# Kernel optimization log

Measured on AMD Instinct MI355X. Metric: run time of the kernel, lower is better.

The kernel has to match this reference:

```python
import jax, jax.numpy as jnp
import numpy as np

HIDDEN = 4096
N_HEADS = 32
N_KV_HEADS = 8
HEAD_DIM = HIDDEN // N_HEADS  # 128
GROUPS = N_HEADS // N_KV_HEADS  # 4
ROPE_BASE = 10000.0
BATCH, SEQ = 1, 2048


def _rope_cos_sin(position_ids, dim, base):
    # position_ids: [b, s] int -> cos/sin [b, s, dim]
    inv_freq = 1.0 / (base ** (jnp.arange(0, dim, 2, dtype=jnp.float32) / dim))  # [dim/2]
    freqs = position_ids.astype(jnp.float32)[..., None] * inv_freq  # [b, s, dim/2]
    emb = jnp.concatenate([freqs, freqs], axis=-1)  # [b, s, dim]
    return jnp.cos(emb), jnp.sin(emb)


def _rotate_half(x):
    x1, x2 = jnp.split(x, 2, axis=-1)
    return jnp.concatenate([-x2, x1], axis=-1)


def setup_inputs() -> dict:
    key = jax.random.key(0)
    ks = jax.random.split(key, 8)
    s = 0.02
    return {
        'hidden_states': jax.random.normal(ks[0], (BATCH, SEQ, HIDDEN), dtype=jnp.float32),
        'position_ids': jnp.broadcast_to(jnp.arange(SEQ, dtype=jnp.int64), (BATCH, SEQ)),
        'Wq': jax.random.normal(ks[1], (HIDDEN, N_HEADS * HEAD_DIM), dtype=jnp.float32) * s,
        'bq': jax.random.normal(ks[2], (N_HEADS * HEAD_DIM,), dtype=jnp.float32) * s,
        'Wk': jax.random.normal(ks[3], (HIDDEN, N_KV_HEADS * HEAD_DIM), dtype=jnp.float32) * s,
        'bk': jax.random.normal(ks[4], (N_KV_HEADS * HEAD_DIM,), dtype=jnp.float32) * s,
        'Wv': jax.random.normal(ks[5], (HIDDEN, N_KV_HEADS * HEAD_DIM), dtype=jnp.float32) * s,
        'bv': jax.random.normal(ks[6], (N_KV_HEADS * HEAD_DIM,), dtype=jnp.float32) * s,
        'Wo': jax.random.normal(ks[7], (HIDDEN, HIDDEN), dtype=jnp.float32) * s,
    }


def reference(hidden_states, position_ids, Wq, bq, Wk, bk, Wv, bv, Wo):
    b, s, _ = hidden_states.shape
    # QKV projections (bias=True for q/k/v per module)
    q = hidden_states @ Wq + bq  # [b, s, H*d]
    k = hidden_states @ Wk + bk  # [b, s, Hk*d]
    v = hidden_states @ Wv + bv  # [b, s, Hk*d]
    q = q.reshape(b, s, N_HEADS, HEAD_DIM)
    k = k.reshape(b, s, N_KV_HEADS, HEAD_DIM)
    v = v.reshape(b, s, N_KV_HEADS, HEAD_DIM)

    # RoPE gathered by position_ids
    cos, sin = _rope_cos_sin(position_ids, HEAD_DIM, ROPE_BASE)  # [b, s, d]
    cos = cos[:, :, None, :]
    sin = sin[:, :, None, :]
    q = q * cos + _rotate_half(q) * sin
    k = k * cos + _rotate_half(k) * sin

    # GQA causal attention: group query heads over shared kv heads
    qg = q.reshape(b, s, N_KV_HEADS, GROUPS, HEAD_DIM)
    scale = 1.0 / jnp.sqrt(jnp.asarray(HEAD_DIM, dtype=q.dtype))
    scores = jnp.einsum('bqhgd,bkhd->bhgqk', qg, k) * scale  # [b, Hk, g, s, s]
    causal = jnp.tril(jnp.ones((s, s), dtype=bool))
    scores = jnp.where(causal, scores, jnp.finfo(scores.dtype).min)
    probs = jax.nn.softmax(scores, axis=-1)
    out = jnp.einsum('bhgqk,bkhd->bqhgd', probs, v)  # [b, s, Hk, g, d]
    out = out.reshape(b, s, HIDDEN)
    return out @ Wo  # o_proj, bias=False
```

## Files before the change

kernel.cpp:

```cpp
#include <hip/hip_runtime.h>
#include <hip/hip_bf16.h>

typedef __hip_bfloat16 bf16;
typedef __attribute__((ext_vector_type(8))) __bf16 bf16x8;
typedef __attribute__((ext_vector_type(4))) float f32x4;

#define SEQ 2048
#define HID 4096
#define NH 32
#define NKV 8
#define HD 128
#define KVDIM 1024
#define QKVN 6144

#define MiB (1024 * 1024)
#define SCALE_LOG2E 0.12751743f

__device__ __forceinline__ void gl_lds16(const void* g, void* lds) {
  __builtin_amdgcn_global_load_lds((const __attribute__((address_space(1))) void*)g,
                                   (__attribute__((address_space(3))) void*)lds,
                                   16, 0, 0);
}

__device__ __forceinline__ float unplo(unsigned u) { return __uint_as_float(u << 16); }
__device__ __forceinline__ float unphi(unsigned u) { return __uint_as_float(u & 0xffff0000u); }
__device__ __forceinline__ unsigned packbf(float a, float b) {
  bf16 t[2] = {__float2bfloat16(a), __float2bfloat16(b)};
  return *reinterpret_cast<unsigned*>(t);
}

__global__ void transpose_all_kernel(const float* __restrict__ Wq, const float* __restrict__ Wk,
                                     const float* __restrict__ Wv, const float* __restrict__ Wo,
                                     bf16* __restrict__ Wqkvt, bf16* __restrict__ Wot,
                                     const float* __restrict__ hidden, bf16* __restrict__ Xb,
                                     const float* __restrict__ bq, const float* __restrict__ bk,
                                     const float* __restrict__ bv, float* __restrict__ bqkv) {
  __shared__ float tile[64][65];
  int t = blockIdx.x;
  int tx = threadIdx.x, ty = threadIdx.y;
  int tid = ty * 64 + tx;
  if (t >= 18432) {
    int i = (t - 18432) * 256 + tid;
    bqkv[i] = (i < HID) ? bq[i] : (i < HID + KVDIM ? bk[i - HID] : bv[i - HID - KVDIM]);
    return;
  }
  if (t >= 10240) {
    int i = ((t - 10240) * 256 + tid) * 4;
    float4 v = *reinterpret_cast<const float4*>(hidden + i);
    bf16 o[4] = {__float2bfloat16(v.x), __float2bfloat16(v.y),
                 __float2bfloat16(v.z), __float2bfloat16(v.w)};
    *reinterpret_cast<short4*>(Xb + i) = *reinterpret_cast<const short4*>(o);
    return;
  }
  const float* in;
  bf16* out;
  int si, xt, yt;
  if (t < 4096)      { in = Wq; out = Wqkvt;                           si = HID;   xt = t & 63; yt = t >> 6; }
  else if (t < 5120) { t -= 4096; in = Wk; out = Wqkvt + (size_t)HID * HID;           si = KVDIM; xt = t & 15; yt = t >> 4; }
  else if (t < 6144) { t -= 5120; in = Wv; out = Wqkvt + (size_t)(HID + KVDIM) * HID; si = KVDIM; xt = t & 15; yt = t >> 4; }
  else               { t -= 6144; in = Wo; out = Wot;                 si = HID;   xt = t & 63; yt = t >> 6; }
  int c0 = xt * 64, r0 = yt * 64;
#pragma unroll
  for (int i = 0; i < 64; i += 4)
    tile[ty + i][tx] = in[(size_t)(r0 + ty + i) * si + (c0 + tx)];
  __syncthreads();
#pragma unroll
  for (int i = 0; i < 64; i += 4)
    out[(size_t)(c0 + ty + i) * HID + (r0 + tx)] = __float2bfloat16(tile[tx][ty + i]);
}

__global__ void postqkv_kernel(const bf16* __restrict__ Ch, bf16* __restrict__ Qb,
                               bf16* __restrict__ Kb, bf16* __restrict__ Vt) {
  __shared__ float tile[32][33];
  int b = blockIdx.x;
  int tid = threadIdx.x;
  if (b < 10240) {
    bool isQ = (b < 8192);
    int idx = (isQ ? b : b - 8192) * 256 + tid;
    int j = idx & 31;
    int h = (idx >> 5) & (isQ ? 31 : 7);
    int s = idx >> (isQ ? 10 : 8);
    size_t bi = (size_t)s * QKVN + (isQ ? 0 : HID) + h * HD;
    unsigned u1 = *reinterpret_cast<const unsigned*>(Ch + bi + 2 * j);
    unsigned u2 = *reinterpret_cast<const unsigned*>(Ch + bi + 64 + 2 * j);
    float x1a = unplo(u1), x1b = unphi(u1);
    float x2a = unplo(u2), x2b = unphi(u2);
    float inv0 = __expf(-(float)(2 * j) * 0.14391156831212787f);
    float inv1 = __expf(-(float)(2 * j + 1) * 0.14391156831212787f);
    float sn0, cs0, sn1, cs1;
    __sincosf((float)s * inv0, &sn0, &cs0);
    __sincosf((float)s * inv1, &sn1, &cs1);
    if (isQ) {
      cs0 *= SCALE_LOG2E; sn0 *= SCALE_LOG2E;
      cs1 *= SCALE_LOG2E; sn1 *= SCALE_LOG2E;
    }
    size_t bo = (size_t)s * (isQ ? HID : KVDIM) + h * HD;
    bf16* Ob = isQ ? Qb : Kb;
    *reinterpret_cast<unsigned*>(Ob + bo + 2 * j) =
        packbf(x1a * cs0 - x2a * sn0, x1b * cs1 - x2b * sn1);
    *reinterpret_cast<unsigned*>(Ob + bo + 64 + 2 * j) =
        packbf(x2a * cs0 + x1a * sn0, x2b * cs1 + x1b * sn1);
  } else {
    int t = b - 10240;
    int xt = t & 31, yt = t >> 5;
    int tx = tid & 31, ty = tid >> 5;
#pragma unroll
    for (int i = 0; i < 32; i += 8)
      tile[ty + i][tx] = __bfloat162float(Ch[(size_t)(yt * 32 + ty + i) * QKVN + (HID + KVDIM) + xt * 32 + tx]);
    __syncthreads();
#pragma unroll
    for (int i = 0; i < 32; i += 8)
      Vt[(size_t)(xt * 32 + ty + i) * SEQ + (yt * 32 + tx)] = __float2bfloat16(tile[tx][ty + i]);
  }
}

#define BARRIER() __builtin_amdgcn_s_barrier()
#define MFMA_ACC(d, x, y) d = __builtin_amdgcn_mfma_f32_16x16x32_bf16(x, y, d, 0, 0, 0)

__global__ __launch_bounds__(512, 2) void qkvgemm_kernel(
    const bf16* __restrict__ A,
    const bf16* __restrict__ Bt,
    const float* __restrict__ bias,
    bf16* __restrict__ Ch) {
  __shared__ bf16 lds[2][448 * 64];
  const int blk = blockIdx.x;
  const int xcd = blk & 7, loc = blk >> 3;
  const int bx = xcd * 4 + (loc & 3);
  const int by = loc >> 2;
  const int n0 = bx * 192;
  const int m0 = by * 256;
  const int tid = threadIdx.x;
  const int lane = tid & 63;
  const int w = tid >> 6;
  const int wr = w >> 2, wc = w & 3;
  const int hig = lane >> 4;
  const int nt = HID / 64;

#define QSTAGE_A(buf, t)                                                          \
  {                                                                               \
    _Pragma("unroll")                                                             \
    for (int _c = 0; _c < 4; ++_c) {                                              \
      int _row = _c * 64 + w * 8 + (lane >> 3);                                   \
      int _ch = (lane & 7) ^ ((lane >> 3) & 7);                                   \
      gl_lds16(A + (size_t)(m0 + _row) * HID + (size_t)(t) * 64 + _ch * 8,        \
               &lds[buf][(_c * 64 + w * 8) * 64]);                                \
    }                                                                             \
  }
#define QSTAGE_B(buf, t)                                                          \
  {                                                                               \
    _Pragma("unroll")                                                             \
    for (int _c = 0; _c < 3; ++_c) {                                              \
      int _row = _c * 64 + w * 8 + (lane >> 3);                                   \
      int _ch = (lane & 7) ^ ((lane >> 3) & 7);                                   \
      gl_lds16(Bt + (size_t)(n0 + _row) * HID + (size_t)(t) * 64 + _ch * 8,       \
               &lds[buf][(256 + _c * 64 + w * 8) * 64]);                          \
    }                                                                             \
  }

  auto rdA = [&](int cur, int mi, int ks) {
    int rr = wr * 128 + mi * 16 + (lane & 15);
    int byt = rr * 128 + (((ks * 32 + hig * 8) * 2) ^ ((rr & 7) << 4));
    return *reinterpret_cast<const bf16x8*>(
        reinterpret_cast<const char*>(&lds[cur][0]) + byt);
  };
  auto rdB = [&](int cur, int ni, int ks) {
    int rr = wc * 48 + ni * 16 + (lane & 15);
    int byt = 32768 + rr * 128 + (((ks * 32 + hig * 8) * 2) ^ ((rr & 7) << 4));
    return *reinterpret_cast<const bf16x8*>(
        reinterpret_cast<const char*>(&lds[cur][0]) + byt);
  };

  f32x4 acc[8][3];
  const f32x4 z = {0.f, 0.f, 0.f, 0.f};
#pragma unroll
  for (int i = 0; i < 8; ++i)
#pragma unroll
    for (int j = 0; j < 3; ++j) acc[i][j] = z;

  QSTAGE_A(0, 0); QSTAGE_B(0, 0);
  QSTAGE_B(1, 1);
  asm volatile("s_waitcnt vmcnt(3)" ::: "memory");
  BARRIER();

  bf16x8 a[4][2], b[3][2];
  int cur = 0;
  for (int t = 0; t < nt; ++t, cur ^= 1) {
#pragma unroll
    for (int mi = 0; mi < 4; ++mi) { a[mi][0] = rdA(cur, mi, 0); a[mi][1] = rdA(cur, mi, 1); }
#pragma unroll
    for (int ni = 0; ni < 3; ++ni) { b[ni][0] = rdB(cur, ni, 0); b[ni][1] = rdB(cur, ni, 1); }
    if (t + 1 < nt) QSTAGE_A(cur ^ 1, t + 1);
    __builtin_amdgcn_s_setprio(1);
#pragma unroll
    for (int mi = 0; mi < 4; ++mi)
#pragma unroll
      for (int ni = 0; ni < 3; ++ni) {
        MFMA_ACC(acc[mi][ni], a[mi][0], b[ni][0]);
        MFMA_ACC(acc[mi][ni], a[mi][1], b[ni][1]);
      }
    __builtin_amdgcn_s_setprio(0);
    BARRIER();
#pragma unroll
    for (int mi = 0; mi < 4; ++mi) { a[mi][0] = rdA(cur, mi + 4, 0); a[mi][1] = rdA(cur, mi + 4, 1); }
    if (t + 2 < nt) QSTAGE_B(cur, t + 2);
    __builtin_amdgcn_s_setprio(1);
#pragma unroll
    for (int mi = 0; mi < 4; ++mi)
#pragma unroll
      for (int ni = 0; ni < 3; ++ni) {
        MFMA_ACC(acc[mi + 4][ni], a[mi][0], b[ni][0]);
        MFMA_ACC(acc[mi + 4][ni], a[mi][1], b[ni][1]);
      }
    __builtin_amdgcn_s_setprio(0);
    if (t + 1 < nt) {
      if (t + 2 < nt) {
        asm volatile("s_waitcnt vmcnt(3)" ::: "memory");
      } else {
        asm volatile("s_waitcnt vmcnt(0)" ::: "memory");
      }
    }
    BARRIER();
  }

#pragma unroll
  for (int ni = 0; ni < 3; ++ni) {
    int col = n0 + wc * 48 + ni * 16 + (lane & 15);
    float bv = bias[col];
#pragma unroll
    for (int mi = 0; mi < 8; ++mi) {
      int rbase = m0 + wr * 128 + mi * 16 + hig * 4;
#pragma unroll
      for (int r = 0; r < 4; ++r)
        Ch[(size_t)(rbase + r) * QKVN + col] = __float2bfloat16(acc[mi][ni][r] + bv);
    }
  }
#undef QSTAGE_A
#undef QSTAGE_B
}

__global__ __launch_bounds__(512, 2) void wogemm_kernel(
    const bf16* __restrict__ A,
    const bf16* __restrict__ Bt,
    float* __restrict__ C) {
  __shared__ bf16 lds[2][3][128 * 64];
  const int blk = blockIdx.x;
  const int xcd = blk & 7, loc = blk >> 3;
  const int n0 = (xcd * 4 + (loc & 3)) * 128;
  const int m0 = (loc >> 2) * 256;
  const int tid = threadIdx.x;
  const int lane = tid & 63;
  const int w = tid >> 6;
  const int wr = w >> 1, wc = w & 1;
  const int nt = HID / 64;

#define WSTAGE(buf, slot, t)                                                    \
  {                                                                             \
    const bf16* _s = ((slot) == 2) ? Bt : A;                                    \
    int _g0 = ((slot) == 2) ? n0 : (m0 + (slot) * 128);                         \
    _Pragma("unroll")                                                           \
    for (int _it = 0; _it < 2; ++_it) {                                         \
      int _row = w * 16 + _it * 8 + (lane >> 3);                                \
      int _ch = (lane & 7) ^ (_row & 7);                                        \
      gl_lds16(_s + (size_t)(_g0 + _row) * HID + (size_t)(t) * 64 + _ch * 8,    \
               &lds[buf][slot][(w * 16 + _it * 8) * 64]);                       \
    }                                                                           \
  }

  auto rdA = [&](int cur, int mi, int ks) {
    int rr = (wr & 1) * 64 + mi * 16 + (lane & 15);
    int byt = rr * 128 + (((ks * 32 + (lane >> 4) * 8) * 2) ^ ((rr & 7) << 4));
    return *reinterpret_cast<const bf16x8*>(
        reinterpret_cast<const char*>(&lds[cur][wr >> 1][0]) + byt);
  };
  auto rdB = [&](int cur, int ni, int ks) {
    int rr = wc * 64 + ni * 16 + (lane & 15);
    int byt = rr * 128 + (((ks * 32 + (lane >> 4) * 8) * 2) ^ ((rr & 7) << 4));
    return *reinterpret_cast<const bf16x8*>(
        reinterpret_cast<const char*>(&lds[cur][2][0]) + byt);
  };

  f32x4 acc[4][4];
  const f32x4 z = {0.f, 0.f, 0.f, 0.f};
#pragma unroll
  for (int i = 0; i < 4; ++i)
#pragma unroll
    for (int j = 0; j < 4; ++j) acc[i][j] = z;

  WSTAGE(0, 0, 0); WSTAGE(0, 1, 0); WSTAGE(0, 2, 0);
  WSTAGE(1, 2, 1);
  asm volatile("s_waitcnt vmcnt(2)" ::: "memory");
  BARRIER();

  bf16x8 a[2][2], b[4][2];
  int cur = 0;
  for (int t = 0; t < nt; ++t, cur ^= 1) {
#pragma unroll
    for (int mi = 0; mi < 2; ++mi) { a[mi][0] = rdA(cur, mi, 0); a[mi][1] = rdA(cur, mi, 1); }
#pragma unroll
    for (int ni = 0; ni < 4; ++ni) { b[ni][0] = rdB(cur, ni, 0); b[ni][1] = rdB(cur, ni, 1); }
    if (t + 1 < nt) { WSTAGE(cur ^ 1, 0, t + 1); WSTAGE(cur ^ 1, 1, t + 1); }
    __builtin_amdgcn_s_setprio(1);
#pragma unroll
    for (int mi = 0; mi < 2; ++mi)
#pragma unroll
      for (int ni = 0; ni < 4; ++ni) {
        MFMA_ACC(acc[mi][ni], a[mi][0], b[ni][0]);
        MFMA_ACC(acc[mi][ni], a[mi][1], b[ni][1]);
      }
    __builtin_amdgcn_s_setprio(0);
    BARRIER();
#pragma unroll
    for (int mi = 0; mi < 2; ++mi) { a[mi][0] = rdA(cur, mi + 2, 0); a[mi][1] = rdA(cur, mi + 2, 1); }
    if (t + 2 < nt) WSTAGE(cur, 2, t + 2);
    __builtin_amdgcn_s_setprio(1);
#pragma unroll
    for (int mi = 0; mi < 2; ++mi)
#pragma unroll
      for (int ni = 0; ni < 4; ++ni) {
        MFMA_ACC(acc[mi + 2][ni], a[mi][0], b[ni][0]);
        MFMA_ACC(acc[mi + 2][ni], a[mi][1], b[ni][1]);
      }
    __builtin_amdgcn_s_setprio(0);
    if (t + 1 < nt) {
      if (t + 2 < nt) {
        asm volatile("s_waitcnt vmcnt(2)" ::: "memory");
      } else {
        asm volatile("s_waitcnt vmcnt(0)" ::: "memory");
      }
    }
    BARRIER();
  }

#pragma unroll
  for (int ni = 0; ni < 4; ++ni) {
    int col = n0 + wc * 64 + ni * 16 + (lane & 15);
#pragma unroll
    for (int mi = 0; mi < 4; ++mi) {
      int rbase = m0 + wr * 64 + mi * 16 + (lane >> 4) * 4;
#pragma unroll
      for (int r = 0; r < 4; ++r)
        C[(size_t)(rbase + r) * HID + col] = acc[mi][ni][r];
    }
  }
#undef WSTAGE
}

__global__ __launch_bounds__(256) void attn_kernel(
    const bf16* __restrict__ Q, const bf16* __restrict__ Kb,
    const bf16* __restrict__ Vt, bf16* __restrict__ AO) {
  __shared__ bf16 Ks[64 * 128];
  __shared__ bf16 Vs[128 * 64];
  __shared__ bf16 Ps[4][16 * 64];
  const int tid = threadIdx.x, lane = tid & 63, w = tid >> 6;
  const int b = blockIdx.x;
  const int H = b & 31;
  const int pr = b >> 5;
  const int kvh = H >> 2;
  const int hig = lane >> 4;
  const int q_loc = lane & 15;
  const f32x4 z = {0.f, 0.f, 0.f, 0.f};

#pragma unroll
  for (int pass = 0; pass < 2; ++pass) {
    const int qb = pass ? (31 - pr) : pr;
    const int qw = qb * 64 + w * 16;
    const int qa = qw + q_loc;

    bf16x8 aq[4];
#pragma unroll
    for (int kd = 0; kd < 4; ++kd) {
      int row = qw + q_loc;
      int d = kd * 32 + hig * 8;
      aq[kd] = *reinterpret_cast<const bf16x8*>(Q + (size_t)row * HID + H * HD + d);
    }

    float m_run = -1e30f, l_run = 0.0f;
    f32x4 o[8];
#pragma unroll
    for (int dt = 0; dt < 8; ++dt) o[dt] = z;

    for (int t = 0; t <= qb; ++t) {
      int kvbase = t * 64;
#pragma unroll
      for (int it = 0; it < 4; ++it) {
        int c = w * 4 + it;
        int row = c * 4 + (lane >> 4);
        int sb = ((lane & 15) * 16) ^ ((row & 7) << 4);
        gl_lds16(Kb + (size_t)(kvbase + row) * KVDIM + kvh * HD + (sb >> 1), &Ks[c * 512]);
      }
#pragma unroll
      for (int it = 0; it < 4; ++it) {
        int c = w * 4 + it;
        int row = c * 8 + (lane >> 3);
        int sb = ((lane & 7) * 16) ^ ((row & 7) << 4);
        gl_lds16(Vt + (size_t)(kvh * HD + row) * SEQ + kvbase + (sb >> 1), &Vs[c * 512]);
      }
      __syncthreads();

      f32x4 sf[4];
#pragma unroll
      for (int j = 0; j < 4; ++j) sf[j] = z;
#pragma unroll
      for (int j = 0; j < 4; ++j) {
#pragma unroll
        for (int kd = 0; kd < 4; ++kd) {
          int r = j * 16 + q_loc;
          int byt = r * 256 + (((kd * 32 + hig * 8) * 2) ^ ((r & 7) << 4));
          bf16x8 kfr = *reinterpret_cast<const bf16x8*>(reinterpret_cast<const char*>(Ks) + byt);
          sf[j] = __builtin_amdgcn_mfma_f32_16x16x32_bf16(kfr, aq[kd], sf[j], 0, 0, 0);
        }
      }

      float vals[4][4];
      bool diag = (t == qb);
#pragma unroll
      for (int j = 0; j < 4; ++j)
#pragma unroll
        for (int r = 0; r < 4; ++r) {
          float v = sf[j][r];
          if (diag) {
            int ka = kvbase + j * 16 + hig * 4 + r;
            if (ka > qa) v = -1e30f;
          }
          vals[j][r] = v;
        }

      float m01 = fmaxf(fmaxf(vals[0][0], vals[0][1]), fmaxf(vals[0][2], vals[0][3]));
      float m23 = fmaxf(fmaxf(vals[1][0], vals[1][1]), fmaxf(vals[1][2], vals[1][3]));
      float m45 = fmaxf(fmaxf(vals[2][0], vals[2][1]), fmaxf(vals[2][2], vals[2][3]));
      float m67 = fmaxf(fmaxf(vals[3][0], vals[3][1]), fmaxf(vals[3][2], vals[3][3]));
      float m = fmaxf(fmaxf(m01, m23), fmaxf(m45, m67));
      m = fmaxf(m, __shfl_xor(m, 16));
      m = fmaxf(m, __shfl_xor(m, 32));
      float m_old = m_run;
      float mn = fmaxf(m_old, m);
      m_run = mn;
      float alpha = __builtin_exp2f(m_old - mn);

      float p[4][4];
      float rs = 0.0f;
#pragma unroll
      for (int j = 0; j < 4; ++j)
#pragma unroll
        for (int r = 0; r < 4; ++r) {
          p[j][r] = __builtin_exp2f(vals[j][r] - mn);
          rs += p[j][r];
        }
      rs += __shfl_xor(rs, 16);
      rs += __shfl_xor(rs, 32);
      l_run = l_run * alpha + rs;

#pragma unroll
      for (int j = 0; j < 4; ++j) {
        bf16 tmp[4] = {__float2bfloat16(p[j][0]), __float2bfloat16(p[j][1]),
                       __float2bfloat16(p[j][2]), __float2bfloat16(p[j][3])};
        int coff = (j * 16 + hig * 4) * 2;
        int byt = q_loc * 128 + (coff ^ ((q_loc & 7) << 4));
        *reinterpret_cast<uint2*>(reinterpret_cast<char*>(&Ps[w][0]) + byt) =
            *reinterpret_cast<const uint2*>(tmp);
      }

      if (__any(mn > m_old)) {
#pragma unroll
        for (int r = 0; r < 4; ++r) {
          float alr = __shfl(alpha, hig * 4 + r);
#pragma unroll
          for (int dt = 0; dt < 8; ++dt) o[dt][r] *= alr;
        }
      }

      bf16x8 pa[2];
#pragma unroll
      for (int ks = 0; ks < 2; ++ks) {
        int byt = q_loc * 128 + (((ks * 32 + hig * 8) * 2) ^ ((q_loc & 7) << 4));
        pa[ks] = *reinterpret_cast<const bf16x8*>(reinterpret_cast<const char*>(&Ps[w][0]) + byt);
      }
#pragma unroll
      for (int dt = 0; dt < 8; ++dt)
#pragma unroll
        for (int ks = 0; ks < 2; ++ks) {
          int vrow = dt * 16 + q_loc;
          int byt = vrow * 128 + (((ks * 32 + hig * 8) * 2) ^ ((vrow & 7) << 4));
          bf16x8 vb = *reinterpret_cast<const bf16x8*>(reinterpret_cast<const char*>(Vs) + byt);
          o[dt] = __builtin_amdgcn_mfma_f32_16x16x32_bf16(pa[ks], vb, o[dt], 0, 0, 0);
        }
      __syncthreads();
    }

#pragma unroll
    for (int r = 0; r < 4; ++r) {
      float li = __shfl(l_run, hig * 4 + r);
      float linv = 1.0f / li;
#pragma unroll
      for (int dt = 0; dt < 8; ++dt) {
        int qrow = qw + hig * 4 + r;
        int d = dt * 16 + q_loc;
        AO[(size_t)qrow * HID + H * HD + d] = __float2bfloat16(o[dt][r] * linv);
      }
    }
  }
}

extern "C" void kernel_launch(void* const* d_in, const int* in_sizes, int n_in,
                              void* d_out, int out_size, void* d_ws, size_t ws_size,
                              hipStream_t stream) {
  const float* hidden = (const float*)d_in[0];
  const float* Wq = (const float*)d_in[2];
  const float* bq = (const float*)d_in[3];
  const float* Wk = (const float*)d_in[4];
  const float* bk = (const float*)d_in[5];
  const float* Wv = (const float*)d_in[6];
  const float* bv = (const float*)d_in[7];
  const float* Wo = (const float*)d_in[8];
  float* out = (float*)d_out;

  char* ws = (char*)d_ws;
  bf16*  Wqkvt  = (bf16*)(ws + (size_t)0 * MiB);
  bf16*  Xb     = (bf16*)(ws + (size_t)48 * MiB);
  bf16*  Cqkvh  = (bf16*)(ws + (size_t)64 * MiB);
  bf16*  Wot    = (bf16*)(ws + (size_t)88 * MiB);
  bf16*  Qb     = (bf16*)(ws + (size_t)120 * MiB);
  bf16*  Kb     = (bf16*)(ws + (size_t)136 * MiB);
  bf16*  Vt     = (bf16*)(ws + (size_t)140 * MiB);
  float* bqkv   = (float*)Qb;
  bf16*  AO     = Cqkvh;

  transpose_all_kernel<<<18456, dim3(64, 4), 0, stream>>>(
      Wq, Wk, Wv, Wo, Wqkvt, Wot, hidden, Xb, bq, bk, bv, bqkv);

  qkvgemm_kernel<<<256, 512, 0, stream>>>(Xb, Wqkvt, bqkv, Cqkvh);

  postqkv_kernel<<<12288, 256, 0, stream>>>(Cqkvh, Qb, Kb, Vt);

  attn_kernel<<<512, 256, 0, stream>>>(Qb, Kb, Vt, AO);

  wogemm_kernel<<<256, 512, 0, stream>>>(AO, Wot, out);
}
```

Baseline: 296.8 us.

## Triple-buffer B tiles in GEMM kernels to drop mid-iteration barrier

Both projection GEMMs split shared memory into a double-buffered A region and a triple-buffered B region. With B staged two tiles ahead into its own third slot, the barrier between the two MFMA halves of each k-step is removed, leaving one barrier per iteration. The barrier on the last iteration is also skipped. This raises LDS usage per block (qkv: about 136KB instead of 112KB), which may limit blocks per CU despite launch bounds of 2.

```diff
diff --git a/kernel.cpp b/kernel.cpp
--- a/kernel.cpp
+++ b/kernel.cpp
@@ -122,7 +122,8 @@
     const bf16* __restrict__ Bt,
     const float* __restrict__ bias,
     bf16* __restrict__ Ch) {
-  __shared__ bf16 lds[2][448 * 64];
+  __shared__ bf16 ldsA[2][256 * 64];
+  __shared__ bf16 ldsB[3][192 * 64];
   const int blk = blockIdx.x;
   const int xcd = blk & 7, loc = blk >> 3;
   const int bx = xcd * 4 + (loc & 3);
@@ -143,7 +144,7 @@
       int _row = _c * 64 + w * 8 + (lane >> 3);                                   \
       int _ch = (lane & 7) ^ ((lane >> 3) & 7);                                   \
       gl_lds16(A + (size_t)(m0 + _row) * HID + (size_t)(t) * 64 + _ch * 8,        \
-               &lds[buf][(_c * 64 + w * 8) * 64]);                                \
+               &ldsA[buf][(_c * 64 + w * 8) * 64]);                               \
     }                                                                             \
   }
 #define QSTAGE_B(buf, t)                                                          \
@@ -153,21 +154,21 @@
       int _row = _c * 64 + w * 8 + (lane >> 3);                                   \
       int _ch = (lane & 7) ^ ((lane >> 3) & 7);                                   \
       gl_lds16(Bt + (size_t)(n0 + _row) * HID + (size_t)(t) * 64 + _ch * 8,       \
-               &lds[buf][(256 + _c * 64 + w * 8) * 64]);                          \
+               &ldsB[buf][(_c * 64 + w * 8) * 64]);                               \
     }                                                                             \
   }
 
-  auto rdA = [&](int cur, int mi, int ks) {
+  auto rdA = [&](int ca, int mi, int ks) {
     int rr = wr * 128 + mi * 16 + (lane & 15);
     int byt = rr * 128 + (((ks * 32 + hig * 8) * 2) ^ ((rr & 7) << 4));
     return *reinterpret_cast<const bf16x8*>(
-        reinterpret_cast<const char*>(&lds[cur][0]) + byt);
+        reinterpret_cast<const char*>(&ldsA[ca][0]) + byt);
   };
-  auto rdB = [&](int cur, int ni, int ks) {
+  auto rdB = [&](int cb, int ni, int ks) {
     int rr = wc * 48 + ni * 16 + (lane & 15);
-    int byt = 32768 + rr * 128 + (((ks * 32 + hig * 8) * 2) ^ ((rr & 7) << 4));
+    int byt = rr * 128 + (((ks * 32 + hig * 8) * 2) ^ ((rr & 7) << 4));
     return *reinterpret_cast<const bf16x8*>(
-        reinterpret_cast<const char*>(&lds[cur][0]) + byt);
+        reinterpret_cast<const char*>(&ldsB[cb][0]) + byt);
   };
 
   f32x4 acc[8][3];
@@ -183,13 +184,14 @@
   BARRIER();
 
   bf16x8 a[4][2], b[3][2];
-  int cur = 0;
-  for (int t = 0; t < nt; ++t, cur ^= 1) {
-#pragma unroll
-    for (int mi = 0; mi < 4; ++mi) { a[mi][0] = rdA(cur, mi, 0); a[mi][1] = rdA(cur, mi, 1); }
-#pragma unroll
-    for (int ni = 0; ni < 3; ++ni) { b[ni][0] = rdB(cur, ni, 0); b[ni][1] = rdB(cur, ni, 1); }
-    if (t + 1 < nt) QSTAGE_A(cur ^ 1, t + 1);
+  for (int t = 0; t < nt; ++t) {
+    const int ca = t & 1;
+    const int cb = t % 3;
+#pragma unroll
+    for (int mi = 0; mi < 4; ++mi) { a[mi][0] = rdA(ca, mi, 0); a[mi][1] = rdA(ca, mi, 1); }
+#pragma unroll
+    for (int ni = 0; ni < 3; ++ni) { b[ni][0] = rdB(cb, ni, 0); b[ni][1] = rdB(cb, ni, 1); }
+    if (t + 1 < nt) QSTAGE_A((t + 1) & 1, t + 1);
     __builtin_amdgcn_s_setprio(1);
 #pragma unroll
     for (int mi = 0; mi < 4; ++mi)
@@ -199,10 +201,9 @@
         MFMA_ACC(acc[mi][ni], a[mi][1], b[ni][1]);
       }
     __builtin_amdgcn_s_setprio(0);
-    BARRIER();
-#pragma unroll
-    for (int mi = 0; mi < 4; ++mi) { a[mi][0] = rdA(cur, mi + 4, 0); a[mi][1] = rdA(cur, mi + 4, 1); }
-    if (t + 2 < nt) QSTAGE_B(cur, t + 2);
+#pragma unroll
+    for (int mi = 0; mi < 4; ++mi) { a[mi][0] = rdA(ca, mi + 4, 0); a[mi][1] = rdA(ca, mi + 4, 1); }
+    if (t + 2 < nt) QSTAGE_B((t + 2) % 3, t + 2);
     __builtin_amdgcn_s_setprio(1);
 #pragma unroll
     for (int mi = 0; mi < 4; ++mi)
@@ -218,8 +219,8 @@
       } else {
         asm volatile("s_waitcnt vmcnt(0)" ::: "memory");
       }
-    }
-    BARRIER();
+      BARRIER();
+    }
   }
 
 #pragma unroll
@@ -242,7 +243,8 @@
     const bf16* __restrict__ A,
     const bf16* __restrict__ Bt,
     float* __restrict__ C) {
-  __shared__ bf16 lds[2][3][128 * 64];
+  __shared__ bf16 ldsA[2][256 * 64];
+  __shared__ bf16 ldsB[3][128 * 64];
   const int blk = blockIdx.x;
   const int xcd = blk & 7, loc = blk >> 3;
   const int n0 = (xcd * 4 + (loc & 3)) * 128;
@@ -251,32 +253,41 @@
   const int lane = tid & 63;
   const int w = tid >> 6;
   const int wr = w >> 1, wc = w & 1;
+  const int hig = lane >> 4;
   const int nt = HID / 64;
 
-#define WSTAGE(buf, slot, t)                                                    \
-  {                                                                             \
-    const bf16* _s = ((slot) == 2) ? Bt : A;                                    \
-    int _g0 = ((slot) == 2) ? n0 : (m0 + (slot) * 128);                         \
-    _Pragma("unroll")                                                           \
-    for (int _it = 0; _it < 2; ++_it) {                                         \
-      int _row = w * 16 + _it * 8 + (lane >> 3);                                \
-      int _ch = (lane & 7) ^ (_row & 7);                                        \
-      gl_lds16(_s + (size_t)(_g0 + _row) * HID + (size_t)(t) * 64 + _ch * 8,    \
-               &lds[buf][slot][(w * 16 + _it * 8) * 64]);                       \
-    }                                                                           \
-  }
-
-  auto rdA = [&](int cur, int mi, int ks) {
-    int rr = (wr & 1) * 64 + mi * 16 + (lane & 15);
-    int byt = rr * 128 + (((ks * 32 + (lane >> 4) * 8) * 2) ^ ((rr & 7) << 4));
+#define WSTAGE_A(buf, t)                                                          \
+  {                                                                               \
+    _Pragma("unroll")                                                             \
+    for (int _c = 0; _c < 4; ++_c) {                                              \
+      int _row = _c * 64 + w * 8 + (lane >> 3);                                   \
+      int _ch = (lane & 7) ^ ((lane >> 3) & 7);                                   \
+      gl_lds16(A + (size_t)(m0 + _row) * HID + (size_t)(t) * 64 + _ch * 8,        \
+               &ldsA[buf][(_c * 64 + w * 8) * 64]);                               \
+    }                                                                             \
+  }
+#define WSTAGE_B(buf, t)                                                          \
+  {                                                                               \
+    _Pragma("unroll")                                                             \
+    for (int _c = 0; _c < 2; ++_c) {                                              \
+      int _row = _c * 64 + w * 8 + (lane >> 3);                                   \
+      int _ch = (lane & 7) ^ ((lane >> 3) & 7);                                   \
+      gl_lds16(Bt + (size_t)(n0 + _row) * HID + (size_t)(t) * 64 + _ch * 8,       \
+               &ldsB[buf][(_c * 64 + w * 8) * 64]);                               \
+    }                                                                             \
+  }
+
+  auto rdA = [&](int ca, int mi, int ks) {
+    int rr = wr * 64 + mi * 16 + (lane & 15);
+    int byt = rr * 128 + (((ks * 32 + hig * 8) * 2) ^ ((rr & 7) << 4));
     return *reinterpret_cast<const bf16x8*>(
-        reinterpret_cast<const char*>(&lds[cur][wr >> 1][0]) + byt);
+        reinterpret_cast<const char*>(&ldsA[ca][0]) + byt);
   };
-  auto rdB = [&](int cur, int ni, int ks) {
+  auto rdB = [&](int cb, int ni, int ks) {
     int rr = wc * 64 + ni * 16 + (lane & 15);
-    int byt = rr * 128 + (((ks * 32 + (lane >> 4) * 8) * 2) ^ ((rr & 7) << 4));
+    int byt = rr * 128 + (((ks * 32 + hig * 8) * 2) ^ ((rr & 7) << 4));
     return *reinterpret_cast<const bf16x8*>(
-        reinterpret_cast<const char*>(&lds[cur][2][0]) + byt);
+        reinterpret_cast<const char*>(&ldsB[cb][0]) + byt);
   };
 
   f32x4 acc[4][4];
@@ -286,19 +297,20 @@
 #pragma unroll
     for (int j = 0; j < 4; ++j) acc[i][j] = z;
 
-  WSTAGE(0, 0, 0); WSTAGE(0, 1, 0); WSTAGE(0, 2, 0);
-  WSTAGE(1, 2, 1);
+  WSTAGE_A(0, 0); WSTAGE_B(0, 0);
+  WSTAGE_B(1, 1);
   asm volatile("s_waitcnt vmcnt(2)" ::: "memory");
   BARRIER();
 
   bf16x8 a[2][2], b[4][2];
-  int cur = 0;
-  for (int t = 0; t < nt; ++t, cur ^= 1) {
-#pragma unroll
-    for (int mi = 0; mi < 2; ++mi) { a[mi][0] = rdA(cur, mi, 0); a[mi][1] = rdA(cur, mi, 1); }
-#pragma unroll
-    for (int ni = 0; ni < 4; ++ni) { b[ni][0] = rdB(cur, ni, 0); b[ni][1] = rdB(cur, ni, 1); }
-    if (t + 1 < nt) { WSTAGE(cur ^ 1, 0, t + 1); WSTAGE(cur ^ 1, 1, t + 1); }
+  for (int t = 0; t < nt; ++t) {
+    const int ca = t & 1;
+    const int cb = t % 3;
+#pragma unroll
+    for (int mi = 0; mi < 2; ++mi) { a[mi][0] = rdA(ca, mi, 0); a[mi][1] = rdA(ca, mi, 1); }
+#pragma unroll
+    for (int ni = 0; ni < 4; ++ni) { b[ni][0] = rdB(cb, ni, 0); b[ni][1] = rdB(cb, ni, 1); }
+    if (t + 1 < nt) WSTAGE_A((t + 1) & 1, t + 1);
     __builtin_amdgcn_s_setprio(1);
 #pragma unroll
     for (int mi = 0; mi < 2; ++mi)
@@ -308,10 +320,9 @@
         MFMA_ACC(acc[mi][ni], a[mi][1], b[ni][1]);
       }
     __builtin_amdgcn_s_setprio(0);
-    BARRIER();
-#pragma unroll
-    for (int mi = 0; mi < 2; ++mi) { a[mi][0] = rdA(cur, mi + 2, 0); a[mi][1] = rdA(cur, mi + 2, 1); }
-    if (t + 2 < nt) WSTAGE(cur, 2, t + 2);
+#pragma unroll
+    for (int mi = 0; mi < 2; ++mi) { a[mi][0] = rdA(ca, mi + 2, 0); a[mi][1] = rdA(ca, mi + 2, 1); }
+    if (t + 2 < nt) WSTAGE_B((t + 2) % 3, t + 2);
     __builtin_amdgcn_s_setprio(1);
 #pragma unroll
     for (int mi = 0; mi < 2; ++mi)
@@ -327,8 +338,8 @@
       } else {
         asm volatile("s_waitcnt vmcnt(0)" ::: "memory");
       }
-    }
-    BARRIER();
+      BARRIER();
+    }
   }
 
 #pragma unroll
@@ -336,13 +347,14 @@
     int col = n0 + wc * 64 + ni * 16 + (lane & 15);
 #pragma unroll
     for (int mi = 0; mi < 4; ++mi) {
-      int rbase = m0 + wr * 64 + mi * 16 + (lane >> 4) * 4;
+      int rbase = m0 + wr * 64 + mi * 16 + hig * 4;
 #pragma unroll
       for (int r = 0; r < 4; ++r)
         C[(size_t)(rbase + r) * HID + col] = acc[mi][ni][r];
     }
   }
-#undef WSTAGE
+#undef WSTAGE_A
+#undef WSTAGE_B
 }
 
 __global__ __launch_bounds__(256) void attn_kernel(
```

After: 297.9 us. About the same (+0.3%).
